# Kernel tuning notes

Measured on AMD Instinct MI355X. Metric: run time of the kernel, lower is better.

## Reference

```python
import jax, jax.numpy as jnp
import numpy as np

B, T, V = 16, 2048, 512


def setup_inputs() -> dict:
    key = jax.random.key(0)
    k1, k2, k3, k4 = jax.random.split(key, 4)
    idx = jax.random.randint(k1, (B, T), 0, V)
    # torch init: normal(mean=0.1, std=0.02)
    pos_table = 0.1 + 0.02 * jax.random.normal(k2, (T, 1), dtype=jnp.float32)
    Wq = 0.1 + 0.02 * jax.random.normal(k3, (V, V), dtype=jnp.float32)
    Wv = 0.1 + 0.02 * jax.random.normal(k4, (V, V), dtype=jnp.float32)
    return {"idx": idx, "pos_table": pos_table, "Wq": Wq, "Wv": Wv}


def reference(idx, pos_table, Wq, Wv):
    # e = one_hot token embedding: (B, T, V)
    e = jax.nn.one_hot(idx, Wq.shape[0], dtype=pos_table.dtype)
    t = idx.shape[1]
    # relative positions, clamped at 0 (pos[pos<0]=0 in torch)
    pos = jnp.arange(t)
    rel = jnp.maximum(pos[:, None] - pos[None, :], 0)  # (T, T) int
    pe = pos_table[rel, 0]  # (T, T)
    causal = jnp.tril(jnp.ones((t, t), dtype=bool))
    # layer one (Wk falsy branch): einsum('BTe,Tt->BTt', e, pe).tril() @ e
    a1 = jnp.where(causal, jnp.einsum('btv,ts->bts', e, pe), 0.0)  # (B,T,T)
    l1 = a1 @ e  # (B, T, V)
    # layer two (Wk truthy branch; note Wk weight is never applied in fwd):
    # (Wq(e) @ l1^T).tril() @ Wv(e)
    Q = e @ Wq.T   # (B, T, V)
    Vv = e @ Wv.T  # (B, T, V)
    a2 = jnp.where(causal, jnp.einsum('btv,bsv->bts', Q, l1), 0.0)  # (B,T,T)
    logits = a2 @ Vv  # (B, T, V)
    return logits
```

## Files before the change

### kernel.cpp

```cpp
#include <hip/hip_runtime.h>
#include <hip/hip_bf16.h>
#include <math.h>

#define BB 16
#define TT 2048
#define VV 512

typedef __attribute__((ext_vector_type(8))) short short8;
typedef __attribute__((ext_vector_type(4))) float floatx4;

static __device__ inline ushort f2bf(float f) {
  __hip_bfloat16 h = __float2bfloat16(f);
  return *(ushort*)&h;
}

static __device__ __forceinline__ void cp16(const void* g, void* l) {
  __builtin_amdgcn_global_load_lds((const __attribute__((address_space(1))) void*)g,
                                   (__attribute__((address_space(3))) void*)l, 16, 0, 0);
}

static __device__ __forceinline__ void balance_map(int y, int z, int* t_t, int* b) {
  const int r = y & 3, q = z >> 2;
  int t = (q == 0) ? r : (q == 1) ? (r + 8) : (q == 2) ? (7 - r) : (15 - r);
  *t_t = t;
  *b = ((z & 3) << 2) | (y >> 2);
}


__global__ __launch_bounds__(256) void k_transpose_wq(const float* __restrict__ Wq,
                                                      ushort* __restrict__ WqT) {
  int u = blockIdx.x;
  for (int v = threadIdx.x; v < VV; v += blockDim.x)
    WqT[u * VV + v] = f2bf(Wq[(size_t)v * VV + u]);
}

__global__ __launch_bounds__(256) void k_build_pe(const float* __restrict__ h,
                                                  ushort* __restrict__ PE) {
  int t = blockIdx.x;
  ushort* out = PE + (size_t)t * TT;
  for (int p = threadIdx.x; p < TT; p += blockDim.x)
    out[p] = (p <= t) ? f2bf(h[t - p]) : (ushort)0;
}

__global__ __launch_bounds__(256) void k_build_mv(const int* __restrict__ idx,
                                                  const float* __restrict__ Wv,
                                                  const ushort* __restrict__ WqT,
                                                  ushort* __restrict__ M,
                                                  ushort* __restrict__ VvT) {
  int bv = blockIdx.x;
  int b = bv >> 9, v = bv & (VV - 1);
  __shared__ float wrow[VV];
  __shared__ ushort qrow[VV];
  for (int u = threadIdx.x; u < VV; u += blockDim.x) {
    wrow[u] = Wv[(size_t)v * VV + u];
    qrow[u] = WqT[(size_t)v * VV + u];
  }
  __syncthreads();
  const int* row = idx + b * TT;
  ushort* om = M + (size_t)bv * TT;
  ushort* ov = VvT + (size_t)bv * TT;
  for (int s4 = threadIdx.x * 4; s4 < TT; s4 += blockDim.x * 4) {
    int4 iv = *(const int4*)(row + s4);
    ushort4 m, w;
    m.x = qrow[iv.x];  w.x = f2bf(wrow[iv.x]);
    m.y = qrow[iv.y];  w.y = f2bf(wrow[iv.y]);
    m.z = qrow[iv.z];  w.z = f2bf(wrow[iv.z]);
    m.w = qrow[iv.w];  w.w = f2bf(wrow[iv.w]);
    *(ushort4*)(om + s4) = m;
    *(ushort4*)(ov + s4) = w;
  }
}


#define GEMM_PRELUDE()                                                         \
  __shared__ __attribute__((aligned(16))) short As[2 * 128 * 32];              \
  __shared__ __attribute__((aligned(16))) short Bs[2 * 128 * 32];              \
  const int tid = threadIdx.x;                                                 \
  const int lane = tid & 63;                                                   \
  const int wm = (tid >> 6) & 1, wn = tid >> 7;                                \
  const int quad = lane >> 4, ln = lane & 15;                                  \
  const int rr = tid >> 2;                                                     \
  const int cg = (((tid & 3) ^ (rr & 3)) << 3);                                \
  short* a_dst = &As[tid * 8];                                                 \
  short* b_dst = &Bs[tid * 8];                                                 \
  const short* ap[4];                                                          \
  const short* bp[4];                                                          \
  _Pragma("unroll") for (int i = 0; i < 4; i++)                                \
      ap[i] = &As[(wm * 64 + i * 16 + ln) * 32 + ((quad ^ (ln & 3)) << 3)];    \
  _Pragma("unroll") for (int j = 0; j < 4; j++)                                \
      bp[j] = &Bs[(wn * 64 + j * 16 + ln) * 32 + ((quad ^ (ln & 3)) << 3)];

#define GEMM_STAGE(c, PA0, PA1, PB0, PB1)                                      \
  {                                                                            \
    const int _o = (c) << 12;                    \
    cp16((PA0), a_dst + _o);                                                   \
    cp16((PA1), a_dst + _o + 2048);                                            \
    cp16((PB0), b_dst + _o);                                                   \
    cp16((PB1), b_dst + _o + 2048);                                            \
  }

#define GEMM_COMPUTE(c)                                                        \
  {                                                                            \
    const int _o = (c) << 12;                                                  \
    short8 af[4], bfr[4];                                                      \
    _Pragma("unroll") for (int i = 0; i < 4; i++)                              \
        af[i] = *(const short8*)(ap[i] + _o);                                  \
    _Pragma("unroll") for (int j = 0; j < 4; j++)                              \
        bfr[j] = *(const short8*)(bp[j] + _o);                                 \
    _Pragma("unroll") for (int i = 0; i < 4; i++)                              \
        _Pragma("unroll") for (int j = 0; j < 4; j++)                          \
            acc[i][j] = __builtin_amdgcn_mfma_f32_16x16x32_bf16(               \
                af[i], bfr[j], acc[i][j], 0, 0, 0);                            \
  }

#define ZERO_ACC()                                                             \
  _Pragma("unroll") for (int i = 0; i < 4; i++)                                \
      _Pragma("unroll") for (int j = 0; j < 4; j++)                            \
          acc[i][j] = (floatx4){0.f, 0.f, 0.f, 0.f};

__global__ __launch_bounds__(256) void k_gemm_gt(const ushort* __restrict__ M,
                                                 const ushort* __restrict__ PE,
                                                 ushort* __restrict__ GT) {
  int s_t, b;
  balance_map(blockIdx.y, blockIdx.z, &s_t, &b);
  const int u_t = blockIdx.x;
  const int u0 = u_t << 7, s0 = s_t << 7;
  const int nk = (s_t << 2) + 4;
  GEMM_PRELUDE();
  const ushort* a_src0 = M + ((size_t)((b << 9) + u0 + rr)) * TT + cg;
  const ushort* a_src1 = a_src0 + (size_t)64 * TT;
  const ushort* b_src0 = PE + (size_t)(s0 + rr) * TT + cg;
  const ushort* b_src1 = b_src0 + (size_t)64 * TT;
  floatx4 acc[4][4];
  ZERO_ACC();
  GEMM_STAGE(0, a_src0, a_src1, b_src0, b_src1);
  __syncthreads();
  int cur = 0;
#pragma unroll 1
  for (int kt = 0; kt < nk; ++kt) {
    if (kt + 1 < nk) {
      const int ko = (kt + 1) << 5;
      GEMM_STAGE(cur ^ 1, a_src0 + ko, a_src1 + ko, b_src0 + ko, b_src1 + ko);
    }
    GEMM_COMPUTE(cur);
    __syncthreads();
    cur ^= 1;
  }
#pragma unroll
  for (int i = 0; i < 4; i++)
#pragma unroll
    for (int j = 0; j < 4; j++) {
      const int rowb = u0 + wm * 64 + i * 16 + quad * 4;
      const int col = s0 + wn * 64 + j * 16 + ln;
#pragma unroll
      for (int r = 0; r < 4; r++)
        GT[((size_t)((b << 9) + rowb + r)) * TT + col] = f2bf(acc[i][j][r]);
    }
}

__global__ __launch_bounds__(256) void k_diag(const int* __restrict__ idx,
                                              const ushort* __restrict__ GT,
                                              ushort* __restrict__ a2d) {
  const int t_t = blockIdx.x, b = blockIdx.y;
  const int t0 = t_t << 7;
  ushort* outt = a2d + (((size_t)(b << 4) + t_t) << 14);
  for (int e = threadIdx.x; e < 2048; e += 256) {
    const int r = e >> 4;
    const int c8 = (e & 15) << 3;
    const int u = idx[(b << 11) + t0 + r];
    const ushort* src = GT + ((size_t)((b << 9) + u)) * TT + t0 + c8;
    ushort4 lo = *(const ushort4*)(src);
    ushort4 hi = *(const ushort4*)(src + 4);
    ushort vals[8] = {lo.x, lo.y, lo.z, lo.w, hi.x, hi.y, hi.z, hi.w};
    ushort o[8];
#pragma unroll
    for (int k = 0; k < 8; ++k) o[k] = (c8 + k <= r) ? vals[k] : (ushort)0;
    *(ushort4*)(outt + r * 128 + c8) = *(ushort4*)&o[0];
    *(ushort4*)(outt + r * 128 + c8 + 4) = *(ushort4*)&o[4];
  }
}

__global__ __launch_bounds__(256) void k_gemm2(const int* __restrict__ idx,
                                               const ushort* __restrict__ GT,
                                               const ushort* __restrict__ a2d,
                                               const ushort* __restrict__ VvT,
                                               float* __restrict__ out) {
  int t_t, b;
  balance_map(blockIdx.y, blockIdx.z, &t_t, &b);
  const int j_t = blockIdx.x;
  const int t0 = t_t << 7, j0 = j_t << 7;
  const int nk_main = t_t << 2;
  const int nk = nk_main + 4;
  GEMM_PRELUDE();
  const int u0 = idx[(b << 11) + t0 + rr];
  const int u1 = idx[(b << 11) + t0 + rr + 64];
  const ushort* a_src0 = GT + ((size_t)(b << 9) + u0) * TT + cg;
  const ushort* a_src1 = GT + ((size_t)(b << 9) + u1) * TT + cg;
  const ushort* b_src0 = VvT + ((size_t)((b << 9) + j0 + rr)) * TT + cg;
  const ushort* b_src1 = b_src0 + (size_t)64 * TT;
  const ushort* ad0 = a2d + (((size_t)(b << 4) + t_t) << 14) + (size_t)rr * 128 + cg;
  const ushort* ad1 = ad0 + (size_t)64 * 128;
#define A0_AT(kt) ((kt) < nk_main ? a_src0 + ((kt) << 5) : ad0 + (((kt) - nk_main) << 5))
#define A1_AT(kt) ((kt) < nk_main ? a_src1 + ((kt) << 5) : ad1 + (((kt) - nk_main) << 5))
  floatx4 acc[4][4];
  ZERO_ACC();
  GEMM_STAGE(0, A0_AT(0), A1_AT(0), b_src0, b_src1);
  __syncthreads();
  int cur = 0;
#pragma unroll 1
  for (int kt = 0; kt < nk; ++kt) {
    if (kt + 1 < nk) {
      const int ko = (kt + 1) << 5;
      GEMM_STAGE(cur ^ 1, A0_AT(kt + 1), A1_AT(kt + 1), b_src0 + ko, b_src1 + ko);
    }
    GEMM_COMPUTE(cur);
    __syncthreads();
    cur ^= 1;
  }
#undef A0_AT
#undef A1_AT
#pragma unroll
  for (int i = 0; i < 4; i++)
#pragma unroll
    for (int j = 0; j < 4; j++) {
      const int rowb = t0 + wm * 64 + i * 16 + quad * 4;
      const int col = j0 + wn * 64 + j * 16 + ln;
#pragma unroll
      for (int r = 0; r < 4; r++)
        out[((size_t)((b << 11) + rowb + r)) * VV + col] = acc[i][j][r];
    }
}

extern "C" void kernel_launch(void* const* d_in, const int* in_sizes, int n_in,
                              void* d_out, int out_size, void* d_ws, size_t ws_size,
                              hipStream_t stream) {
  const int* idx = (const int*)d_in[0];
  const float* pos_table = (const float*)d_in[1];
  const float* Wq = (const float*)d_in[2];
  const float* Wv = (const float*)d_in[3];
  float* out = (float*)d_out;

  char* ws = (char*)d_ws;
  ushort* WqT = (ushort*)(ws);
  ushort* PE = (ushort*)(ws + 524288UL);
  ushort* M = (ushort*)(ws + 8912896UL);
  ushort* VvT = (ushort*)(ws + 42467328UL);
  ushort* GT = (ushort*)(ws + 76021760UL);
  ushort* a2d = (ushort*)(ws + 109576192UL);

  k_transpose_wq<<<dim3(VV), 256, 0, stream>>>(Wq, WqT);
  k_build_pe<<<dim3(TT), 256, 0, stream>>>(pos_table, PE);
  k_build_mv<<<dim3(BB * VV), 256, 0, stream>>>(idx, Wv, WqT, M, VvT);
  k_gemm_gt<<<dim3(4, 16, BB), 256, 0, stream>>>(M, PE, GT);
  k_diag<<<dim3(16, BB), 256, 0, stream>>>(idx, GT, a2d);
  k_gemm2<<<dim3(4, 16, BB), 256, 0, stream>>>(idx, GT, a2d, VvT, out);
}
```

Measured before the change: 225.6 us.

## Use triple-buffered LDS pipeline with explicit vmcnt waits and longest-first tile order

Both GEMM kernels move from a double-buffered loop with __syncthreads to a three-stage LDS ring that prefetches two K-tiles ahead. Each step waits on vmcnt for only the oldest stage, uses raw s_barrier around the compute, and raises wave priority during the MFMAs. This is meant to hide more global-load latency. The balance_map block mapping is replaced by launching the longest causal tiles first, a simple longest-first schedule. In exchange LDS use grows by half, which may lower occupancy, and correctness now depends on the hand-written vmcnt counts.

```diff
diff --git a/kernel.cpp b/kernel.cpp
--- a/kernel.cpp
+++ b/kernel.cpp
@@ -17,13 +17,6 @@
 static __device__ __forceinline__ void cp16(const void* g, void* l) {
   __builtin_amdgcn_global_load_lds((const __attribute__((address_space(1))) void*)g,
                                    (__attribute__((address_space(3))) void*)l, 16, 0, 0);
-}
-
-static __device__ __forceinline__ void balance_map(int y, int z, int* t_t, int* b) {
-  const int r = y & 3, q = z >> 2;
-  int t = (q == 0) ? r : (q == 1) ? (r + 8) : (q == 2) ? (7 - r) : (15 - r);
-  *t_t = t;
-  *b = ((z & 3) << 2) | (y >> 2);
 }
 
 
@@ -73,8 +66,8 @@
 
 
 #define GEMM_PRELUDE()                                                         \
-  __shared__ __attribute__((aligned(16))) short As[2 * 128 * 32];              \
-  __shared__ __attribute__((aligned(16))) short Bs[2 * 128 * 32];              \
+  __shared__ __attribute__((aligned(16))) short As[3 * 128 * 32];              \
+  __shared__ __attribute__((aligned(16))) short Bs[3 * 128 * 32];              \
   const int tid = threadIdx.x;                                                 \
   const int lane = tid & 63;                                                   \
   const int wm = (tid >> 6) & 1, wn = tid >> 7;                                \
@@ -92,7 +85,7 @@
 
 #define GEMM_STAGE(c, PA0, PA1, PB0, PB1)                                      \
   {                                                                            \
-    const int _o = (c) << 12;                    \
+    const int _o = (c) << 12;                        \
     cp16((PA0), a_dst + _o);                                                   \
     cp16((PA1), a_dst + _o + 2048);                                            \
     cp16((PB0), b_dst + _o);                                                   \
@@ -118,11 +111,39 @@
       _Pragma("unroll") for (int j = 0; j < 4; j++)                            \
           acc[i][j] = (floatx4){0.f, 0.f, 0.f, 0.f};
 
+#define PIPE_LOOP(NK, STAGE_AT)                                                \
+  {                                                                            \
+    STAGE_AT(0, 0);                                                            \
+    STAGE_AT(1, 1);                                                            \
+    int cur = 0, pf = 2;                                                       \
+    _Pragma("unroll 1") for (int kt = 0; kt < (NK); ++kt) {                    \
+      if (kt + 2 < (NK)) {                                                     \
+        STAGE_AT(pf, kt + 2);                                                  \
+        asm volatile("s_waitcnt vmcnt(8)" ::: "memory");                       \
+      } else if (kt + 1 < (NK)) {                                              \
+        asm volatile("s_waitcnt vmcnt(4)" ::: "memory");                       \
+      } else {                                                                 \
+        asm volatile("s_waitcnt vmcnt(0)" ::: "memory");                       \
+      }                                                                        \
+      __builtin_amdgcn_sched_barrier(0);                                       \
+      __builtin_amdgcn_s_barrier();                                            \
+      __builtin_amdgcn_sched_barrier(0);                                       \
+      __builtin_amdgcn_s_setprio(1);                                           \
+      GEMM_COMPUTE(cur);                                                       \
+      __builtin_amdgcn_s_setprio(0);                                           \
+      __builtin_amdgcn_sched_barrier(0);                                       \
+      __builtin_amdgcn_s_barrier();                                            \
+      __builtin_amdgcn_sched_barrier(0);                                       \
+      cur = (cur == 2) ? 0 : cur + 1;                                          \
+      pf = (pf == 2) ? 0 : pf + 1;                                             \
+    }                                                                          \
+  }
+
 __global__ __launch_bounds__(256) void k_gemm_gt(const ushort* __restrict__ M,
                                                  const ushort* __restrict__ PE,
                                                  ushort* __restrict__ GT) {
-  int s_t, b;
-  balance_map(blockIdx.y, blockIdx.z, &s_t, &b);
+  const int s_t = 15 - (int)blockIdx.y;
+  const int b = blockIdx.z;
   const int u_t = blockIdx.x;
   const int u0 = u_t << 7, s0 = s_t << 7;
   const int nk = (s_t << 2) + 4;
@@ -133,19 +154,11 @@
   const ushort* b_src1 = b_src0 + (size_t)64 * TT;
   floatx4 acc[4][4];
   ZERO_ACC();
-  GEMM_STAGE(0, a_src0, a_src1, b_src0, b_src1);
-  __syncthreads();
-  int cur = 0;
-#pragma unroll 1
-  for (int kt = 0; kt < nk; ++kt) {
-    if (kt + 1 < nk) {
-      const int ko = (kt + 1) << 5;
-      GEMM_STAGE(cur ^ 1, a_src0 + ko, a_src1 + ko, b_src0 + ko, b_src1 + ko);
-    }
-    GEMM_COMPUTE(cur);
-    __syncthreads();
-    cur ^= 1;
-  }
+#define SA_GT(c, k)                                                            \
+  GEMM_STAGE(c, a_src0 + ((k) << 5), a_src1 + ((k) << 5), b_src0 + ((k) << 5), \
+             b_src1 + ((k) << 5))
+  PIPE_LOOP(nk, SA_GT);
+#undef SA_GT
 #pragma unroll
   for (int i = 0; i < 4; i++)
 #pragma unroll
@@ -185,8 +198,8 @@
                                                const ushort* __restrict__ a2d,
                                                const ushort* __restrict__ VvT,
                                                float* __restrict__ out) {
-  int t_t, b;
-  balance_map(blockIdx.y, blockIdx.z, &t_t, &b);
+  const int t_t = 15 - (int)blockIdx.y;
+  const int b = blockIdx.z;
   const int j_t = blockIdx.x;
   const int t0 = t_t << 7, j0 = j_t << 7;
   const int nk_main = t_t << 2;
@@ -200,25 +213,15 @@
   const ushort* b_src1 = b_src0 + (size_t)64 * TT;
   const ushort* ad0 = a2d + (((size_t)(b << 4) + t_t) << 14) + (size_t)rr * 128 + cg;
   const ushort* ad1 = ad0 + (size_t)64 * 128;
-#define A0_AT(kt) ((kt) < nk_main ? a_src0 + ((kt) << 5) : ad0 + (((kt) - nk_main) << 5))
-#define A1_AT(kt) ((kt) < nk_main ? a_src1 + ((kt) << 5) : ad1 + (((kt) - nk_main) << 5))
   floatx4 acc[4][4];
   ZERO_ACC();
-  GEMM_STAGE(0, A0_AT(0), A1_AT(0), b_src0, b_src1);
-  __syncthreads();
-  int cur = 0;
-#pragma unroll 1
-  for (int kt = 0; kt < nk; ++kt) {
-    if (kt + 1 < nk) {
-      const int ko = (kt + 1) << 5;
-      GEMM_STAGE(cur ^ 1, A0_AT(kt + 1), A1_AT(kt + 1), b_src0 + ko, b_src1 + ko);
-    }
-    GEMM_COMPUTE(cur);
-    __syncthreads();
-    cur ^= 1;
-  }
-#undef A0_AT
-#undef A1_AT
+#define SA_G2(c, k)                                                            \
+  GEMM_STAGE(c,                                                                \
+             (k) < nk_main ? a_src0 + ((k) << 5) : ad0 + (((k) - nk_main) << 5), \
+             (k) < nk_main ? a_src1 + ((k) << 5) : ad1 + (((k) - nk_main) << 5), \
+             b_src0 + ((k) << 5), b_src1 + ((k) << 5))
+  PIPE_LOOP(nk, SA_G2);
+#undef SA_G2
 #pragma unroll
   for (int i = 0; i < 4; i++)
 #pragma unroll
```

New measurement: 247.9 us. +9.9%, slower.
